# Kernel optimization log

Hardware: AMD Instinct MI355X
Metric: run time of the kernel (lower is better)

## Reference

```python
import jax, jax.numpy as jnp
import numpy as np

MARGIN = 0.3

def setup_inputs() -> dict:
    key = jax.random.key(0)
    k1, k2 = jax.random.split(key)
    embeddings = jax.random.normal(k1, (8192, 512), dtype=jnp.float32)
    labels = jax.random.randint(k2, (8192,), 0, 128, dtype=jnp.int64)
    return {"embeddings": embeddings, "labels": labels}

def _pairwise_euclidean(x):
    # ||xi - xj|| via GEMM, matching torch reference (relu clamp + sqrt(.+1e-16))
    dot = x @ x.T                      # [B, B]
    sq = jnp.diagonal(dot)             # [B]
    d2 = sq[None, :] - 2.0 * dot + sq[:, None]
    d2 = jnp.maximum(d2, 0.0)
    return jnp.sqrt(d2 + 1e-16)

def reference(embeddings, labels):
    n = embeddings.shape[0]
    d = _pairwise_euclidean(embeddings)                 # [B, B]
    same = labels[:, None] == labels[None, :]           # [B, B]
    eye = jnp.eye(n, dtype=bool)
    mask_pos = same & ~eye
    mask_neg = ~same
    # fused masked row-wise reductions (hard mining)
    hardest_pos = jnp.max(jnp.where(mask_pos, d, -jnp.inf), axis=1)  # [B]
    hardest_neg = jnp.min(jnp.where(mask_neg, d, jnp.inf), axis=1)   # [B]
    valid = mask_pos.any(axis=1) & mask_neg.any(axis=1)              # [B]
    per_row = jax.nn.relu(hardest_pos - hardest_neg + MARGIN)
    per_row = jnp.where(valid, per_row, 0.0)
    denom = jnp.maximum(jnp.sum(valid.astype(per_row.dtype)), 1.0)
    return jnp.sum(per_row) / denom
```

## Files before the change

### kernel.cpp

```cpp
#include <hip/hip_runtime.h>

#define BATCH 8192
#define DIM   512
#define NTILE 1152
#define NFIN  128

typedef __attribute__((ext_vector_type(4))) float  f32x4;
typedef __attribute__((ext_vector_type(8))) __bf16 bf16x8;

__device__ __forceinline__ unsigned short f2bf(float x) {
  unsigned u = __float_as_uint(x);
  u = (u + 0x7FFFu + ((u >> 16) & 1u)) >> 16;
  return (unsigned short)u;
}

__device__ __forceinline__ void load_lds16(const void* g, void* l) {
  __builtin_amdgcn_global_load_lds(
      (__attribute__((address_space(1))) void*)(g),
      (__attribute__((address_space(3))) void*)(l), 16, 0, 0);
}

__device__ __forceinline__ unsigned enc(float f) {
  unsigned u = __float_as_uint(f);
  return u ^ (unsigned)(((int)u >> 31) | 0x80000000);
}
__device__ __forceinline__ float dec(unsigned k) {
  unsigned u = (k & 0x80000000u) ? (k ^ 0x80000000u) : ~k;
  return __uint_as_float(u);
}

__global__ __launch_bounds__(256) void prep_kernel(
    const float* __restrict__ X, unsigned short* __restrict__ Xb,
    float* __restrict__ sq, unsigned* __restrict__ ctrl,
    uint4* __restrict__ pos4, uint4* __restrict__ neg4) {
  int gid = blockIdx.x * 256 + threadIdx.x;
  if (gid == 0) {
    ((float*)ctrl)[0] = 0.f;
    ((float*)ctrl)[1] = 0.f;
    ctrl[2] = 0u;
    ctrl[3] = 0u;
  }
  if (gid < 196608) {
    pos4[gid] = (uint4){0u, 0u, 0u, 0u};
    neg4[gid] = (uint4){~0u, ~0u, ~0u, ~0u};
  }
  int wave = threadIdx.x >> 6, lane = threadIdx.x & 63;
  int row = blockIdx.x * 4 + wave;
  const float4* xr = (const float4*)(X + (size_t)row * DIM);
  float4 a = xr[lane * 2];
  float4 b = xr[lane * 2 + 1];
  float s = a.x*a.x + a.y*a.y + a.z*a.z + a.w*a.w
          + b.x*b.x + b.y*b.y + b.z*b.z + b.w*b.w;
  uint4 p;
  p.x = (unsigned)f2bf(a.x) | ((unsigned)f2bf(a.y) << 16);
  p.y = (unsigned)f2bf(a.z) | ((unsigned)f2bf(a.w) << 16);
  p.z = (unsigned)f2bf(b.x) | ((unsigned)f2bf(b.y) << 16);
  p.w = (unsigned)f2bf(b.z) | ((unsigned)f2bf(b.w) << 16);
  ((uint4*)(Xb + (size_t)row * DIM))[lane] = p;
  #pragma unroll
  for (int off = 32; off > 0; off >>= 1) s += __shfl_down(s, off);
  if (lane == 0) sq[row] = s;
}

template<int NI>
__device__ __forceinline__ void gemm_tile(
    const unsigned short* __restrict__ Xb, int i0, int jw,
    unsigned short* Asm, unsigned short* Bsm,
    int wave, int wm, int wn, int quad, int lc, int rc, int gcol,
    f32x4 (&acc)[4][8]) {
  for (int k0 = 0; k0 < DIM; k0 += 64) {
    #pragma unroll
    for (int tt = 0; tt < 4; tt++) {
      int c = wave * 4 + tt;
      int row = c * 8 + rc;
      load_lds16(Xb + (size_t)(i0 + row) * DIM + k0 + gcol, &Asm[c * 512]);
    }
    #pragma unroll
    for (int tt = 0; tt < NI; tt++) {
      int c = wave * NI + tt;
      int row = c * 8 + rc;
      load_lds16(Xb + (size_t)(jw + row) * DIM + k0 + gcol, &Bsm[c * 512]);
    }
    __syncthreads();
    #pragma unroll
    for (int kk = 0; kk < 64; kk += 32) {
      int kc = kk >> 3;
      int asel = ((kc + quad) ^ (lc & 7)) * 8;
      bf16x8 af[4], bfr[NI];
      #pragma unroll
      for (int mi = 0; mi < 4; mi++)
        af[mi] = *(const bf16x8*)&Asm[(wm * 64 + mi * 16 + lc) * 64 + asel];
      #pragma unroll
      for (int ni = 0; ni < NI; ni++)
        bfr[ni] = *(const bf16x8*)&Bsm[(wn * (NI * 16) + ni * 16 + lc) * 64 + asel];
      __builtin_amdgcn_s_setprio(1);
      #pragma unroll
      for (int mi = 0; mi < 4; mi++)
        #pragma unroll
        for (int ni = 0; ni < NI; ni++)
          acc[mi][ni] = __builtin_amdgcn_mfma_f32_16x16x32_bf16(
              af[mi], bfr[ni], acc[mi][ni], 0, 0, 0);
      __builtin_amdgcn_s_setprio(0);
    }
    __syncthreads();
  }
}

template<bool STRAD, int NI, int WNS>
__device__ __forceinline__ void epilogue(
    const f32x4 (&acc)[4][8], const float* __restrict__ sq,
    const int* __restrict__ labels,
    int i0, int jwin, int wm, int wn, int quad, int lc,
    unsigned (*ibuf)[128][2], unsigned (*jbuf)[256][2]) {
  float sqj_r[NI]; int labj_r[NI];
  #pragma unroll
  for (int ni = 0; ni < NI; ni++) {
    int j = jwin + wn * WNS + ni * 16 + lc;
    sqj_r[ni] = sq[j]; labj_r[ni] = labels[j];
  }
  float rpos[16], rneg[16];
  float jp[NI], jn[NI];
  #pragma unroll
  for (int x = 0; x < NI; x++) { jp[x] = -3e38f; jn[x] = 3e38f; }
  #pragma unroll
  for (int mi = 0; mi < 4; mi++) {
    #pragma unroll
    for (int r = 0; r < 4; r++) {
      int ig = i0 + wm * 64 + mi * 16 + quad * 4 + r;
      int li = labels[ig];
      float si = sq[ig];
      float rp = -3e38f, rn = 3e38f;
      #pragma unroll
      for (int ni = 0; ni < NI; ni++) {
        float a = acc[mi][ni][r];
        float v = fmaf(-2.f, a, sqj_r[ni]);
        bool same = (li == labj_r[ni]);
        bool posok = same;
        if (STRAD) posok = same && ((jwin + wn * WNS + ni * 16 + lc) != ig);
        rp = fmaxf(rp, posok ? v : -3e38f);
        rn = fminf(rn, same ? 3e38f : v);
        if (!STRAD) {
          float v2 = fmaf(-2.f, a, si);
          jp[ni] = fmaxf(jp[ni], same ? v2 : -3e38f);
          jn[ni] = fminf(jn[ni], same ? 3e38f : v2);
        }
      }
      rpos[mi * 4 + r] = rp; rneg[mi * 4 + r] = rn;
    }
  }
  #pragma unroll
  for (int m = 1; m <= 8; m <<= 1)
    #pragma unroll
    for (int x = 0; x < 16; x++) {
      rpos[x] = fmaxf(rpos[x], __shfl_xor(rpos[x], m));
      rneg[x] = fminf(rneg[x], __shfl_xor(rneg[x], m));
    }
  if (lc == 0) {
    #pragma unroll
    for (int mi = 0; mi < 4; mi++)
      #pragma unroll
      for (int r = 0; r < 4; r++) {
        int row = wm * 64 + mi * 16 + quad * 4 + r;
        ibuf[wn][row][0] = enc(rpos[mi * 4 + r]);
        ibuf[wn][row][1] = enc(rneg[mi * 4 + r]);
      }
  }
  if (!STRAD) {
    #pragma unroll
    for (int m = 16; m <= 32; m <<= 1)
      #pragma unroll
      for (int x = 0; x < NI; x++) {
        jp[x] = fmaxf(jp[x], __shfl_xor(jp[x], m));
        jn[x] = fminf(jn[x], __shfl_xor(jn[x], m));
      }
    if (quad == 0) {
      #pragma unroll
      for (int ni = 0; ni < NI; ni++) {
        int col = wn * WNS + ni * 16 + lc;
        jbuf[wm][col][0] = enc(jp[ni]);
        jbuf[wm][col][1] = enc(jn[ni]);
      }
    }
  }
}

__global__ __launch_bounds__(256, 2) void triplet_mfma(
    const unsigned short* __restrict__ Xb, const float* __restrict__ sq,
    const int* __restrict__ labels, unsigned* __restrict__ ctrl,
    unsigned* __restrict__ pos_i, unsigned* __restrict__ neg_i,
    unsigned* __restrict__ pos_j, unsigned* __restrict__ neg_j) {
  __shared__ __align__(16) unsigned short Asm[128 * 64];
  __shared__ __align__(16) unsigned short Bsm[256 * 64];
  __shared__ int tshare;

  unsigned (*ibuf)[128][2] = reinterpret_cast<unsigned (*)[128][2]>(&Asm[0]);
  unsigned (*jbuf)[256][2] = reinterpret_cast<unsigned (*)[256][2]>(&Asm[1024]);

  int tid = threadIdx.x;
  int wave = tid >> 6, lane = tid & 63;
  int wm = wave >> 1, wn = wave & 1;
  int quad = lane >> 4, lc = lane & 15;
  int rc = lane >> 3;
  int gcol = ((lane & 7) ^ rc) * 8;

  for (;;) {
    if (tid == 0) tshare = (int)atomicAdd(&ctrl[3], 1u);
    __syncthreads();
    int t = tshare;
    if (t >= NTILE) break;

    int It = 0, Js = 0, q = -1; bool strad = false;
    if (t < 64) { It = t; Js = t >> 1; strad = true; }
    else {
      int u;
      if (t < 1024) u = t - 64;
      else { q = (t - 1024) & 3; u = 960 + ((t - 1024) >> 2); }
      for (int s = 0; s < 64; s++) {
        int c = 31 - (s >> 1);
        if (u < c) { It = s; Js = (s >> 1) + 1 + u; break; }
        u -= c;
      }
    }
    int i0 = It * 128;
    int jw = Js * 256 + (q >= 0 ? q * 64 : 0);

    f32x4 acc[4][8];
    #pragma unroll
    for (int mi = 0; mi < 4; mi++)
      #pragma unroll
      for (int ni = 0; ni < 8; ni++)
        acc[mi][ni] = (f32x4){0.f, 0.f, 0.f, 0.f};

    if (q >= 0) {
      gemm_tile<2>(Xb, i0, jw, Asm, Bsm, wave, wm, wn, quad, lc, rc, gcol, acc);
      epilogue<false, 2, 32>(acc, sq, labels, i0, jw, wm, wn, quad, lc, ibuf, jbuf);
    } else {
      gemm_tile<8>(Xb, i0, jw, Asm, Bsm, wave, wm, wn, quad, lc, rc, gcol, acc);
      if (strad)
        epilogue<true, 8, 128>(acc, sq, labels, i0, jw, wm, wn, quad, lc, ibuf, jbuf);
      else
        epilogue<false, 8, 128>(acc, sq, labels, i0, jw, wm, wn, quad, lc, ibuf, jbuf);
    }
    __syncthreads();

    if (q >= 0) {
      if (tid < 128) {
        unsigned p = max(ibuf[0][tid][0], ibuf[1][tid][0]);
        unsigned n = min(ibuf[0][tid][1], ibuf[1][tid][1]);
        atomicMax(&pos_i[(size_t)Js * BATCH + i0 + tid], p);
        atomicMin(&neg_i[(size_t)Js * BATCH + i0 + tid], n);
      }
      if (tid < 64) {
        unsigned p = max(jbuf[0][tid][0], jbuf[1][tid][0]);
        unsigned n = min(jbuf[0][tid][1], jbuf[1][tid][1]);
        pos_j[(size_t)It * BATCH + jw + tid] = p;
        neg_j[(size_t)It * BATCH + jw + tid] = n;
      }
    } else {
      if (tid < 128) {
        unsigned p = max(ibuf[0][tid][0], ibuf[1][tid][0]);
        unsigned n = min(ibuf[0][tid][1], ibuf[1][tid][1]);
        pos_i[(size_t)Js * BATCH + i0 + tid] = p;
        neg_i[(size_t)Js * BATCH + i0 + tid] = n;
      }
      if (!strad) {
        unsigned p = max(jbuf[0][tid][0], jbuf[1][tid][0]);
        unsigned n = min(jbuf[0][tid][1], jbuf[1][tid][1]);
        pos_j[(size_t)It * BATCH + jw + tid] = p;
        neg_j[(size_t)It * BATCH + jw + tid] = n;
      }
    }
    __syncthreads();
  }
}

__global__ __launch_bounds__(256) void final_kernel(
    const unsigned* __restrict__ pos_i, const unsigned* __restrict__ neg_i,
    const unsigned* __restrict__ pos_j, const unsigned* __restrict__ neg_j,
    const float* __restrict__ sq, unsigned* __restrict__ ctrl,
    float* __restrict__ out) {
  __shared__ unsigned fbuf[4][64][2];
  int wave = threadIdx.x >> 6, lane = threadIdx.x & 63;
  int r = blockIdx.x * 64 + lane;
  unsigned pe = 0u, ne = 0xFFFFFFFFu;
  #pragma unroll
  for (int k = 0; k < 24; k++) {
    int s = wave * 24 + k;
    const unsigned* ps = (s < 32) ? pos_i + (size_t)s * BATCH
                                  : pos_j + (size_t)(s - 32) * BATCH;
    const unsigned* ns = (s < 32) ? neg_i + (size_t)s * BATCH
                                  : neg_j + (size_t)(s - 32) * BATCH;
    pe = max(pe, ps[r]);
    ne = min(ne, ns[r]);
  }
  fbuf[wave][lane][0] = pe;
  fbuf[wave][lane][1] = ne;
  __syncthreads();
  if (wave == 0) {
    pe = max(max(fbuf[0][lane][0], fbuf[1][lane][0]),
             max(fbuf[2][lane][0], fbuf[3][lane][0]));
    ne = min(min(fbuf[0][lane][1], fbuf[1][lane][1]),
             min(fbuf[2][lane][1], fbuf[3][lane][1]));
    float p = dec(pe), n = dec(ne);
    float term = 0.f, cnt = 0.f;
    if (p > -1e37f && n < 1e37f) {
      float si = sq[r];
      float dp = sqrtf(fmaxf(si + p, 0.f) + 1e-16f);
      float dn = sqrtf(fmaxf(si + n, 0.f) + 1e-16f);
      term = fmaxf(dp - dn + 0.3f, 0.f);
      cnt = 1.f;
    }
    #pragma unroll
    for (int off = 32; off > 0; off >>= 1) {
      term += __shfl_down(term, off);
      cnt  += __shfl_down(cnt, off);
    }
    if (lane == 0) {
      atomicAdd((float*)&ctrl[0], term);
      atomicAdd((float*)&ctrl[1], cnt);
      __threadfence();
      unsigned t = atomicAdd(&ctrl[2], 1u);
      if (t == NFIN - 1) {
        float S = atomicAdd((float*)&ctrl[0], 0.f);
        float C = atomicAdd((float*)&ctrl[1], 0.f);
        out[0] = S / fmaxf(C, 1.f);
      }
    }
  }
}

extern "C" void kernel_launch(void* const* d_in, const int* in_sizes, int n_in,
                              void* d_out, int out_size, void* d_ws, size_t ws_size,
                              hipStream_t stream) {
  const float* X      = (const float*)d_in[0];
  const int*   labels = (const int*)d_in[1];
  float* out = (float*)d_out;
  char* ws = (char*)d_ws;

  const size_t SLOT = (size_t)BATCH * 4;
  unsigned short* Xb = (unsigned short*)ws;
  float* sq      = (float*)(ws + (8u << 20));
  unsigned* ctrl = (unsigned*)(ws + (8u << 20) + (32u << 10));
  char*  posb = ws + (8u << 20) + (64u << 10);
  char*  negb = posb + 96 * SLOT;
  unsigned* pos_i = (unsigned*)posb;
  unsigned* pos_j = (unsigned*)(posb + 32 * SLOT);
  unsigned* neg_i = (unsigned*)negb;
  unsigned* neg_j = (unsigned*)(negb + 32 * SLOT);

  prep_kernel<<<BATCH / 4, 256, 0, stream>>>(X, Xb, sq, ctrl,
                                             (uint4*)posb, (uint4*)negb);
  triplet_mfma<<<512, 256, 0, stream>>>(Xb, sq, labels, ctrl,
                                        pos_i, neg_i, pos_j, neg_j);
  final_kernel<<<NFIN, 256, 0, stream>>>(pos_i, neg_i, pos_j, neg_j, sq, ctrl, out);
}
```

Before: 132.7 us.

## Use 256x256 symmetric tiles with 8-wave blocks and double-buffered LDS staging

Enlarges the GEMM tile from 128x256 to 256x256 over the symmetric upper triangle, which halves the tile count and the number of partial-result slots. Blocks grow to 512 threads in a 2x4 wave layout. LDS A/B buffers are double-buffered so the next K slab is prefetched while MFMAs run on the current one, and the final reduction reads fewer slots. The aim is more data reuse per loaded slab, less per-tile overhead, and load latency hidden behind compute. In exchange it uses 128KB of LDS per block, which limits occupancy, adds register pressure from the 8x4 accumulators, and leaves fewer tiles to balance across CUs.

Result: slower. 194.1 us (+46.2%).

```diff
diff --git a/kernel.cpp b/kernel.cpp
--- a/kernel.cpp
+++ b/kernel.cpp
@@ -2,7 +2,7 @@
 
 #define BATCH 8192
 #define DIM   512
-#define NTILE 1152
+#define NTILE 576
 #define NFIN  128
 
 typedef __attribute__((ext_vector_type(4))) float  f32x4;
@@ -40,7 +40,7 @@
     ctrl[2] = 0u;
     ctrl[3] = 0u;
   }
-  if (gid < 196608) {
+  if (gid < 131072) {
     pos4[gid] = (uint4){0u, 0u, 0u, 0u};
     neg4[gid] = (uint4){~0u, ~0u, ~0u, ~0u};
   }
@@ -62,71 +62,95 @@
   if (lane == 0) sq[row] = s;
 }
 
-template<int NI>
+__device__ __forceinline__ void decode_tile(int t, int& I, int& J, int& q, bool& strad) {
+  I = 0; J = 0; q = -1; strad = false;
+  if (t < 32) { I = t; J = t; strad = true; return; }
+  int u;
+  if (t < 512) u = t - 32;
+  else { q = (t - 512) & 3; u = 480 + ((t - 512) >> 2); }
+  for (int s = 0; s < 32; s++) {
+    int c = 31 - s;
+    if (u < c) { I = s; J = s + 1 + u; return; }
+    u -= c;
+  }
+}
+
+template<int NBT>
+__device__ __forceinline__ void stage_slab(
+    const unsigned short* __restrict__ Xb, int i0, int jw, int k0,
+    unsigned short* A, unsigned short* B, int wave, int rc, int gcol) {
+  #pragma unroll
+  for (int tt = 0; tt < 4; tt++) {
+    int c = wave * 4 + tt;
+    int row = c * 8 + rc;
+    load_lds16(Xb + (size_t)(i0 + row) * DIM + k0 + gcol, &A[c * 512]);
+  }
+  #pragma unroll
+  for (int tt = 0; tt < NBT; tt++) {
+    int c = wave * NBT + tt;
+    int row = c * 8 + rc;
+    load_lds16(Xb + (size_t)(jw + row) * DIM + k0 + gcol, &B[c * 512]);
+  }
+}
+
+template<int NI, int NBT>
 __device__ __forceinline__ void gemm_tile(
     const unsigned short* __restrict__ Xb, int i0, int jw,
-    unsigned short* Asm, unsigned short* Bsm,
-    int wave, int wm, int wn, int quad, int lc, int rc, int gcol,
-    f32x4 (&acc)[4][8]) {
-  for (int k0 = 0; k0 < DIM; k0 += 64) {
-    #pragma unroll
-    for (int tt = 0; tt < 4; tt++) {
-      int c = wave * 4 + tt;
-      int row = c * 8 + rc;
-      load_lds16(Xb + (size_t)(i0 + row) * DIM + k0 + gcol, &Asm[c * 512]);
-    }
-    #pragma unroll
-    for (int tt = 0; tt < NI; tt++) {
-      int c = wave * NI + tt;
-      int row = c * 8 + rc;
-      load_lds16(Xb + (size_t)(jw + row) * DIM + k0 + gcol, &Bsm[c * 512]);
-    }
-    __syncthreads();
+    unsigned short (*Ab)[256 * 64], unsigned short (*Bb)[256 * 64],
+    int wave, int wr, int wc, int quad, int lc, int rc, int gcol,
+    f32x4 (&acc)[8][4]) {
+  stage_slab<NBT>(Xb, i0, jw, 0, Ab[0], Bb[0], wave, rc, gcol);
+  __syncthreads();
+  for (int k = 0; k < 8; k++) {
+    int cur = k & 1;
+    if (k < 7)
+      stage_slab<NBT>(Xb, i0, jw, (k + 1) * 64, Ab[cur ^ 1], Bb[cur ^ 1], wave, rc, gcol);
+    __builtin_amdgcn_sched_barrier(0);
     #pragma unroll
     for (int kk = 0; kk < 64; kk += 32) {
       int kc = kk >> 3;
       int asel = ((kc + quad) ^ (lc & 7)) * 8;
-      bf16x8 af[4], bfr[NI];
-      #pragma unroll
-      for (int mi = 0; mi < 4; mi++)
-        af[mi] = *(const bf16x8*)&Asm[(wm * 64 + mi * 16 + lc) * 64 + asel];
+      bf16x8 af[8], bfr[NI];
+      #pragma unroll
+      for (int mi = 0; mi < 8; mi++)
+        af[mi] = *(const bf16x8*)&Ab[cur][(wr * 128 + mi * 16 + lc) * 64 + asel];
       #pragma unroll
       for (int ni = 0; ni < NI; ni++)
-        bfr[ni] = *(const bf16x8*)&Bsm[(wn * (NI * 16) + ni * 16 + lc) * 64 + asel];
+        bfr[ni] = *(const bf16x8*)&Bb[cur][(wc * (NI * 16) + ni * 16 + lc) * 64 + asel];
       __builtin_amdgcn_s_setprio(1);
       #pragma unroll
-      for (int mi = 0; mi < 4; mi++)
+      for (int mi = 0; mi < 8; mi++)
         #pragma unroll
         for (int ni = 0; ni < NI; ni++)
           acc[mi][ni] = __builtin_amdgcn_mfma_f32_16x16x32_bf16(
               af[mi], bfr[ni], acc[mi][ni], 0, 0, 0);
       __builtin_amdgcn_s_setprio(0);
     }
-    __syncthreads();
-  }
-}
-
-template<bool STRAD, int NI, int WNS>
+    if (k < 7) __syncthreads();
+  }
+}
+
+template<bool STRAD, int NI>
 __device__ __forceinline__ void epilogue(
-    const f32x4 (&acc)[4][8], const float* __restrict__ sq,
+    const f32x4 (&acc)[8][4], const float* __restrict__ sq,
     const int* __restrict__ labels,
-    int i0, int jwin, int wm, int wn, int quad, int lc,
-    unsigned (*ibuf)[128][2], unsigned (*jbuf)[256][2]) {
+    int i0, int jw, int wr, int wc, int quad, int lc,
+    unsigned (*ibuf)[256][2], unsigned (*jbuf)[256][2]) {
   float sqj_r[NI]; int labj_r[NI];
   #pragma unroll
   for (int ni = 0; ni < NI; ni++) {
-    int j = jwin + wn * WNS + ni * 16 + lc;
+    int j = jw + wc * (NI * 16) + ni * 16 + lc;
     sqj_r[ni] = sq[j]; labj_r[ni] = labels[j];
   }
-  float rpos[16], rneg[16];
+  float rpos[32], rneg[32];
   float jp[NI], jn[NI];
   #pragma unroll
   for (int x = 0; x < NI; x++) { jp[x] = -3e38f; jn[x] = 3e38f; }
   #pragma unroll
-  for (int mi = 0; mi < 4; mi++) {
+  for (int mi = 0; mi < 8; mi++) {
     #pragma unroll
     for (int r = 0; r < 4; r++) {
-      int ig = i0 + wm * 64 + mi * 16 + quad * 4 + r;
+      int ig = i0 + wr * 128 + mi * 16 + quad * 4 + r;
       int li = labels[ig];
       float si = sq[ig];
       float rp = -3e38f, rn = 3e38f;
@@ -136,7 +160,7 @@
         float v = fmaf(-2.f, a, sqj_r[ni]);
         bool same = (li == labj_r[ni]);
         bool posok = same;
-        if (STRAD) posok = same && ((jwin + wn * WNS + ni * 16 + lc) != ig);
+        if (STRAD) posok = same && ((jw + wc * (NI * 16) + ni * 16 + lc) != ig);
         rp = fmaxf(rp, posok ? v : -3e38f);
         rn = fminf(rn, same ? 3e38f : v);
         if (!STRAD) {
@@ -151,18 +175,18 @@
   #pragma unroll
   for (int m = 1; m <= 8; m <<= 1)
     #pragma unroll
-    for (int x = 0; x < 16; x++) {
+    for (int x = 0; x < 32; x++) {
       rpos[x] = fmaxf(rpos[x], __shfl_xor(rpos[x], m));
       rneg[x] = fminf(rneg[x], __shfl_xor(rneg[x], m));
     }
   if (lc == 0) {
     #pragma unroll
-    for (int mi = 0; mi < 4; mi++)
+    for (int mi = 0; mi < 8; mi++)
       #pragma unroll
       for (int r = 0; r < 4; r++) {
-        int row = wm * 64 + mi * 16 + quad * 4 + r;
-        ibuf[wn][row][0] = enc(rpos[mi * 4 + r]);
-        ibuf[wn][row][1] = enc(rneg[mi * 4 + r]);
+        int row = wr * 128 + mi * 16 + quad * 4 + r;
+        ibuf[wc][row][0] = enc(rpos[mi * 4 + r]);
+        ibuf[wc][row][1] = enc(rneg[mi * 4 + r]);
       }
   }
   if (!STRAD) {
@@ -176,29 +200,29 @@
     if (quad == 0) {
       #pragma unroll
       for (int ni = 0; ni < NI; ni++) {
-        int col = wn * WNS + ni * 16 + lc;
-        jbuf[wm][col][0] = enc(jp[ni]);
-        jbuf[wm][col][1] = enc(jn[ni]);
-      }
-    }
-  }
-}
-
-__global__ __launch_bounds__(256, 2) void triplet_mfma(
+        int col = wc * (NI * 16) + ni * 16 + lc;
+        jbuf[wr][col][0] = enc(jp[ni]);
+        jbuf[wr][col][1] = enc(jn[ni]);
+      }
+    }
+  }
+}
+
+__global__ __launch_bounds__(512, 2) void triplet_mfma(
     const unsigned short* __restrict__ Xb, const float* __restrict__ sq,
     const int* __restrict__ labels, unsigned* __restrict__ ctrl,
     unsigned* __restrict__ pos_i, unsigned* __restrict__ neg_i,
     unsigned* __restrict__ pos_j, unsigned* __restrict__ neg_j) {
-  __shared__ __align__(16) unsigned short Asm[128 * 64];
-  __shared__ __align__(16) unsigned short Bsm[256 * 64];
+  __shared__ __align__(16) unsigned short Ab[2][256 * 64];
+  __shared__ __align__(16) unsigned short Bb[2][256 * 64];
   __shared__ int tshare;
 
-  unsigned (*ibuf)[128][2] = reinterpret_cast<unsigned (*)[128][2]>(&Asm[0]);
-  unsigned (*jbuf)[256][2] = reinterpret_cast<unsigned (*)[256][2]>(&Asm[1024]);
+  unsigned (*ibuf)[256][2] = reinterpret_cast<unsigned (*)[256][2]>(&Ab[0][0]);
+  unsigned (*jbuf)[256][2] = reinterpret_cast<unsigned (*)[256][2]>(&Ab[0][4096]);
 
   int tid = threadIdx.x;
   int wave = tid >> 6, lane = tid & 63;
-  int wm = wave >> 1, wn = wave & 1;
+  int wr = wave >> 2, wc = wave & 3;
   int quad = lane >> 4, lc = lane & 15;
   int rc = lane >> 3;
   int gcol = ((lane & 7) ^ rc) * 8;
@@ -209,65 +233,59 @@
     int t = tshare;
     if (t >= NTILE) break;
 
-    int It = 0, Js = 0, q = -1; bool strad = false;
-    if (t < 64) { It = t; Js = t >> 1; strad = true; }
-    else {
-      int u;
-      if (t < 1024) u = t - 64;
-      else { q = (t - 1024) & 3; u = 960 + ((t - 1024) >> 2); }
-      for (int s = 0; s < 64; s++) {
-        int c = 31 - (s >> 1);
-        if (u < c) { It = s; Js = (s >> 1) + 1 + u; break; }
-        u -= c;
-      }
-    }
-    int i0 = It * 128;
-    int jw = Js * 256 + (q >= 0 ? q * 64 : 0);
-
-    f32x4 acc[4][8];
-    #pragma unroll
-    for (int mi = 0; mi < 4; mi++)
-      #pragma unroll
-      for (int ni = 0; ni < 8; ni++)
+    int I, J, q; bool strad;
+    decode_tile(t, I, J, q, strad);
+    int i0 = I * 256;
+    int jw = J * 256 + (q >= 0 ? q * 64 : 0);
+
+    f32x4 acc[8][4];
+    #pragma unroll
+    for (int mi = 0; mi < 8; mi++)
+      #pragma unroll
+      for (int ni = 0; ni < 4; ni++)
         acc[mi][ni] = (f32x4){0.f, 0.f, 0.f, 0.f};
 
     if (q >= 0) {
-      gemm_tile<2>(Xb, i0, jw, Asm, Bsm, wave, wm, wn, quad, lc, rc, gcol, acc);
-      epilogue<false, 2, 32>(acc, sq, labels, i0, jw, wm, wn, quad, lc, ibuf, jbuf);
+      gemm_tile<1, 1>(Xb, i0, jw, Ab, Bb, wave, wr, wc, quad, lc, rc, gcol, acc);
+      epilogue<false, 1>(acc, sq, labels, i0, jw, wr, wc, quad, lc, ibuf, jbuf);
+    } else if (strad) {
+      gemm_tile<4, 4>(Xb, i0, jw, Ab, Bb, wave, wr, wc, quad, lc, rc, gcol, acc);
+      epilogue<true, 4>(acc, sq, labels, i0, jw, wr, wc, quad, lc, ibuf, jbuf);
     } else {
-      gemm_tile<8>(Xb, i0, jw, Asm, Bsm, wave, wm, wn, quad, lc, rc, gcol, acc);
-      if (strad)
-        epilogue<true, 8, 128>(acc, sq, labels, i0, jw, wm, wn, quad, lc, ibuf, jbuf);
-      else
-        epilogue<false, 8, 128>(acc, sq, labels, i0, jw, wm, wn, quad, lc, ibuf, jbuf);
+      gemm_tile<4, 4>(Xb, i0, jw, Ab, Bb, wave, wr, wc, quad, lc, rc, gcol, acc);
+      epilogue<false, 4>(acc, sq, labels, i0, jw, wr, wc, quad, lc, ibuf, jbuf);
     }
     __syncthreads();
 
     if (q >= 0) {
-      if (tid < 128) {
-        unsigned p = max(ibuf[0][tid][0], ibuf[1][tid][0]);
-        unsigned n = min(ibuf[0][tid][1], ibuf[1][tid][1]);
-        atomicMax(&pos_i[(size_t)Js * BATCH + i0 + tid], p);
-        atomicMin(&neg_i[(size_t)Js * BATCH + i0 + tid], n);
+      if (tid < 256) {
+        unsigned p = max(max(ibuf[0][tid][0], ibuf[1][tid][0]),
+                         max(ibuf[2][tid][0], ibuf[3][tid][0]));
+        unsigned n = min(min(ibuf[0][tid][1], ibuf[1][tid][1]),
+                         min(ibuf[2][tid][1], ibuf[3][tid][1]));
+        atomicMax(&pos_i[(size_t)J * BATCH + i0 + tid], p);
+        atomicMin(&neg_i[(size_t)J * BATCH + i0 + tid], n);
       }
       if (tid < 64) {
         unsigned p = max(jbuf[0][tid][0], jbuf[1][tid][0]);
         unsigned n = min(jbuf[0][tid][1], jbuf[1][tid][1]);
-        pos_j[(size_t)It * BATCH + jw + tid] = p;
-        neg_j[(size_t)It * BATCH + jw + tid] = n;
+        pos_j[(size_t)I * BATCH + jw + tid] = p;
+        neg_j[(size_t)I * BATCH + jw + tid] = n;
       }
     } else {
-      if (tid < 128) {
-        unsigned p = max(ibuf[0][tid][0], ibuf[1][tid][0]);
-        unsigned n = min(ibuf[0][tid][1], ibuf[1][tid][1]);
-        pos_i[(size_t)Js * BATCH + i0 + tid] = p;
-        neg_i[(size_t)Js * BATCH + i0 + tid] = n;
-      }
-      if (!strad) {
-        unsigned p = max(jbuf[0][tid][0], jbuf[1][tid][0]);
-        unsigned n = min(jbuf[0][tid][1], jbuf[1][tid][1]);
-        pos_j[(size_t)It * BATCH + jw + tid] = p;
-        neg_j[(size_t)It * BATCH + jw + tid] = n;
+      if (tid < 256) {
+        unsigned p = max(max(ibuf[0][tid][0], ibuf[1][tid][0]),
+                         max(ibuf[2][tid][0], ibuf[3][tid][0]));
+        unsigned n = min(min(ibuf[0][tid][1], ibuf[1][tid][1]),
+                         min(ibuf[2][tid][1], ibuf[3][tid][1]));
+        pos_i[(size_t)J * BATCH + i0 + tid] = p;
+        neg_i[(size_t)J * BATCH + i0 + tid] = n;
+        if (!strad) {
+          unsigned pj = max(jbuf[0][tid][0], jbuf[1][tid][0]);
+          unsigned nj = min(jbuf[0][tid][1], jbuf[1][tid][1]);
+          pos_j[(size_t)I * BATCH + jw + tid] = pj;
+          neg_j[(size_t)I * BATCH + jw + tid] = nj;
+        }
       }
     }
     __syncthreads();
@@ -284,8 +302,8 @@
   int r = blockIdx.x * 64 + lane;
   unsigned pe = 0u, ne = 0xFFFFFFFFu;
   #pragma unroll
-  for (int k = 0; k < 24; k++) {
-    int s = wave * 24 + k;
+  for (int k = 0; k < 16; k++) {
+    int s = wave * 16 + k;
     const unsigned* ps = (s < 32) ? pos_i + (size_t)s * BATCH
                                   : pos_j + (size_t)(s - 32) * BATCH;
     const unsigned* ns = (s < 32) ? neg_i + (size_t)s * BATCH
@@ -342,7 +360,7 @@
   float* sq      = (float*)(ws + (8u << 20));
   unsigned* ctrl = (unsigned*)(ws + (8u << 20) + (32u << 10));
   char*  posb = ws + (8u << 20) + (64u << 10);
-  char*  negb = posb + 96 * SLOT;
+  char*  negb = posb + 64 * SLOT;
   unsigned* pos_i = (unsigned*)posb;
   unsigned* pos_j = (unsigned*)(posb + 32 * SLOT);
   unsigned* neg_i = (unsigned*)negb;
@@ -350,7 +368,7 @@
 
   prep_kernel<<<BATCH / 4, 256, 0, stream>>>(X, Xb, sq, ctrl,
                                              (uint4*)posb, (uint4*)negb);
-  triplet_mfma<<<512, 256, 0, stream>>>(Xb, sq, labels, ctrl,
+  triplet_mfma<<<256, 512, 0, stream>>>(Xb, sq, labels, ctrl,
                                         pos_i, neg_i, pos_j, neg_j);
   final_kernel<<<NFIN, 256, 0, stream>>>(pos_i, neg_i, pos_j, neg_j, sq, ctrl, out);
 }
```
